# Kernel optimization log

Measured on AMD Instinct MI355X. Metric: run time of the kernel, lower is better.

Reference implementation:

```python
import jax, jax.numpy as jnp
import numpy as np

B, H, S, D = 4, 16, 2048, 64
MASK_FILL = 1e-12  # module quirk: masked scores set to 1e-12, not -inf


def setup_inputs() -> dict:
    key = jax.random.key(0)
    kq, kk, kv, km = jax.random.split(key, 4)
    q = jax.random.normal(kq, (B, H, S, D), dtype=jnp.float32)
    k = jax.random.normal(kk, (B, H, S, D), dtype=jnp.float32)
    v = jax.random.normal(kv, (B, H, S, D), dtype=jnp.float32)
    mask = jax.random.randint(km, (B, 1, 1, S), 0, 2, dtype=jnp.int32)
    return {"q": q, "k": k, "v": v, "mask": mask}


def reference(q, k, v, mask):
    dim = k.shape[-1]
    # scores: [B,H,S,S]
    scores = jnp.einsum('bhid,bhjd->bhij', q, k) * (dim ** -0.5)
    # faithful to masked_fill(mask == 0, 1e-12)
    scores = jnp.where(mask == 0, jnp.asarray(MASK_FILL, scores.dtype), scores)
    attention = jax.nn.softmax(scores, axis=-1)
    output = jnp.einsum('bhij,bhjd->bhid', attention, v)
    return output, attention
```

## Files before the change

### kernel.cpp

```cpp
#include <hip/hip_runtime.h>
#include <hip/hip_bf16.h>

namespace {

constexpr int S = 2048;
constexpr int D = 64;
constexpr float QSCALE = 0.125f * 1.4426950408889634f;

typedef __bf16 bf16x8 __attribute__((ext_vector_type(8)));
typedef float f32x16 __attribute__((ext_vector_type(16)));

#if __has_builtin(__builtin_amdgcn_exp2f)
__device__ __forceinline__ float fexp2(float x) { return __builtin_amdgcn_exp2f(x); }
#else
__device__ __forceinline__ float fexp2(float x) { return exp2f(x); }
#endif

__device__ __forceinline__ bf16x8 cvt8s(float4 a, float4 b, float s) {
    bf16x8 f;
    f[0] = (__bf16)(a.x * s); f[1] = (__bf16)(a.y * s);
    f[2] = (__bf16)(a.z * s); f[3] = (__bf16)(a.w * s);
    f[4] = (__bf16)(b.x * s); f[5] = (__bf16)(b.y * s);
    f[6] = (__bf16)(b.z * s); f[7] = (__bf16)(b.w * s);
    return f;
}
__device__ __forceinline__ bf16x8 cvt8(float4 a, float4 b) {
    bf16x8 f;
    f[0] = (__bf16)a.x; f[1] = (__bf16)a.y;
    f[2] = (__bf16)a.z; f[3] = (__bf16)a.w;
    f[4] = (__bf16)b.x; f[5] = (__bf16)b.y;
    f[6] = (__bf16)b.z; f[7] = (__bf16)b.w;
    return f;
}
__device__ __forceinline__ unsigned int pkbf(float lo, float hi) {
    unsigned int a = (unsigned int)__builtin_bit_cast(unsigned short, (__bf16)lo);
    unsigned int b = (unsigned int)__builtin_bit_cast(unsigned short, (__bf16)hi);
    return a | (b << 16);
}

}

__global__ void __launch_bounds__(256, 4)
attn_fused(const float* __restrict__ qg, const float* __restrict__ kg,
           const float* __restrict__ vg, const int* __restrict__ mg,
           float* __restrict__ og, float* __restrict__ ag)
{
    __shared__ bf16x8 kstage[2][256];
    __shared__ bf16x8 vstage[2][256];
    __shared__ unsigned int mlds[64];

    const int tid  = threadIdx.x;
    const int lane = tid & 63;
    const int w    = tid >> 6;
    const int l31  = lane & 31;
    const int h2   = lane >> 5;

    const int wid = (blockIdx.x & 7) * 128 + (blockIdx.x >> 3);
    const int bh  = wid >> 4;
    const int q0  = ((wid & 15) * 4 + w) * 32;
    const int b   = bh >> 4;

    const float* qrow = qg + ((size_t)bh * S + q0 + l31) * D + 8 * h2;
    const float* vb_  = vg + (size_t)bh * S * D;
    float* att  = ag + (size_t)bh * S * S + (size_t)q0 * S;
    float* orow = og + ((size_t)bh * S + q0) * D;

    const int srow  = tid >> 3;
    const int scol  = tid & 7;
    const int sslot = srow * 8 + (scol ^ (srow & 7));
    const float* ksrc = kg + (size_t)bh * S * D + (size_t)srow * D + scol * 8;
    int kslot[4];
#pragma unroll
    for (int t = 0; t < 4; ++t)
        kslot[t] = l31 * 8 + ((2 * t + h2) ^ (l31 & 7));

    const int vd = tid & 63;
    const int vw = tid >> 6;
    const int vwslot = vd * 4 + (vw ^ ((vd >> 1) & 3));
    const float* vsrc = vb_ + vd;
    int vslot[2][2];
#pragma unroll
    for (int f = 0; f < 2; ++f)
#pragma unroll
        for (int g = 0; g < 2; ++g) {
            const int d = l31 + 32 * g;
            vslot[f][g] = d * 4 + ((2 * f + h2) ^ ((d >> 1) & 3));
        }

    bf16x8 qa[4];
#pragma unroll
    for (int t = 0; t < 4; ++t) {
        const float4* p4 = (const float4*)(qrow + 16 * t);
        qa[t] = cvt8s(p4[0], p4[1], QSCALE);
    }

    if (tid < 64) {
        const int4* mp = (const int4*)(mg + (size_t)b * S + 32 * tid);
        unsigned int bits = 0;
#pragma unroll
        for (int k = 0; k < 8; ++k) {
            int4 m = mp[k];
            bits |= (unsigned int)(m.x != 0) << (4 * k);
            bits |= (unsigned int)(m.y != 0) << (4 * k + 1);
            bits |= (unsigned int)(m.z != 0) << (4 * k + 2);
            bits |= (unsigned int)(m.w != 0) << (4 * k + 3);
        }
        mlds[tid] = bits;
    }

    {
        const float4* p4 = (const float4*)ksrc;
        kstage[0][sslot] = cvt8(p4[0], p4[1]);
        bf16x8 vv;
#pragma unroll
        for (int k = 0; k < 8; ++k)
            vv[k] = (__bf16)vsrc[(size_t)(8 * vw + k) * D];
        vstage[0][vwslot] = vv;
    }
    __syncthreads();

    float ssum = 0.f;
    f32x16 oacc[2];
#pragma unroll
    for (int g = 0; g < 2; ++g)
#pragma unroll
        for (int r = 0; r < 16; ++r) oacc[g][r] = 0.f;

    int cur = 0;
    for (int j0 = 0; j0 < S; j0 += 32) {
        const bool more = (j0 + 32) < S;
        float4 kna{}, knb{};
        float vp[8];
        if (more) {
            const float4* p4 = (const float4*)(ksrc + (size_t)(j0 + 32) * D);
            kna = p4[0]; knb = p4[1];
#pragma unroll
            for (int k = 0; k < 8; ++k)
                vp[k] = vsrc[(size_t)(j0 + 32 + 8 * vw + k) * D];
        }
        const unsigned int mw = mlds[j0 >> 5];

        f32x16 acc;
#pragma unroll
        for (int r = 0; r < 16; ++r) acc[r] = 0.f;
        __builtin_amdgcn_s_setprio(1);
#pragma unroll
        for (int t = 0; t < 4; ++t)
            acc = __builtin_amdgcn_mfma_f32_32x32x16_bf16(kstage[cur][kslot[t]], qa[t], acc, 0, 0, 0);
        __builtin_amdgcn_s_setprio(0);

        const unsigned int mq = mw >> (4 * h2);
        unsigned int pk[8];
#pragma unroll
        for (int qd = 0; qd < 4; ++qd) {
            float pv[4];
#pragma unroll
            for (int i = 0; i < 4; ++i) {
                const float e = fexp2(acc[4 * qd + i]);
                pv[i] = ((mq >> (i + 8 * qd)) & 1) ? e : 1.0f;
                ssum += pv[i];
            }
            pk[2 * qd]     = pkbf(pv[0], pv[1]);
            pk[2 * qd + 1] = pkbf(pv[2], pv[3]);
        }
        asm volatile("v_permlane32_swap_b32 %0, %1" : "+v"(pk[0]), "+v"(pk[2]));
        asm volatile("v_permlane32_swap_b32 %0, %1" : "+v"(pk[1]), "+v"(pk[3]));
        asm volatile("v_permlane32_swap_b32 %0, %1" : "+v"(pk[4]), "+v"(pk[6]));
        asm volatile("v_permlane32_swap_b32 %0, %1" : "+v"(pk[5]), "+v"(pk[7]));
        typedef unsigned int uint4v __attribute__((ext_vector_type(4)));
        uint4v u0 = {pk[0], pk[1], pk[2], pk[3]};
        uint4v u1 = {pk[4], pk[5], pk[6], pk[7]};
        bf16x8 pa[2];
        pa[0] = __builtin_bit_cast(bf16x8, u0);
        pa[1] = __builtin_bit_cast(bf16x8, u1);

        __builtin_amdgcn_s_setprio(1);
#pragma unroll
        for (int f = 0; f < 2; ++f)
#pragma unroll
            for (int g = 0; g < 2; ++g)
                oacc[g] = __builtin_amdgcn_mfma_f32_32x32x16_bf16(pa[f], vstage[cur][vslot[f][g]], oacc[g], 0, 0, 0);
        __builtin_amdgcn_s_setprio(0);

        if (more) {
            kstage[cur ^ 1][sslot] = cvt8(kna, knb);
            bf16x8 vv;
#pragma unroll
            for (int k = 0; k < 8; ++k) vv[k] = (__bf16)vp[k];
            vstage[cur ^ 1][vwslot] = vv;
        }
        __syncthreads();
        cur ^= 1;
    }

    const float inv = 1.0f / (ssum + __shfl_xor(ssum, 32));
    float invq[16];
#pragma unroll
    for (int r = 0; r < 16; ++r)
        invq[r] = __shfl(inv, (r & 3) + 8 * (r >> 2) + 4 * h2);

#pragma unroll
    for (int g = 0; g < 2; ++g)
#pragma unroll
        for (int r = 0; r < 16; ++r) {
            const int qr = (r & 3) + 8 * (r >> 2) + 4 * h2;
            __builtin_nontemporal_store(oacc[g][r] * invq[r],
                                        &orow[(size_t)qr * D + 32 * g + l31]);
        }

    {
        const float4* p4 = (const float4*)ksrc;
        kstage[0][sslot] = cvt8(p4[0], p4[1]);
    }
    __syncthreads();

    cur = 0;
    for (int j0 = 0; j0 < S; j0 += 32) {
        const bool more = (j0 + 32) < S;
        float4 kna{}, knb{};
        if (more) {
            const float4* p4 = (const float4*)(ksrc + (size_t)(j0 + 32) * D);
            kna = p4[0]; knb = p4[1];
        }
        const bool mf = (mlds[j0 >> 5] >> l31) & 1;

        f32x16 acc;
#pragma unroll
        for (int r = 0; r < 16; ++r) acc[r] = 0.f;
        __builtin_amdgcn_s_setprio(1);
#pragma unroll
        for (int t = 0; t < 4; ++t)
            acc = __builtin_amdgcn_mfma_f32_32x32x16_bf16(qa[t], kstage[cur][kslot[t]], acc, 0, 0, 0);
        __builtin_amdgcn_s_setprio(0);

#pragma unroll
        for (int r = 0; r < 16; ++r) {
            float p = mf ? fexp2(acc[r]) : 1.0f;
            p *= invq[r];
            const int qr = (r & 3) + 8 * (r >> 2) + 4 * h2;
            __builtin_nontemporal_store(p, &att[(size_t)qr * S + j0 + l31]);
        }
        if (more) kstage[cur ^ 1][sslot] = cvt8(kna, knb);
        __syncthreads();
        cur ^= 1;
    }
}

extern "C" void kernel_launch(void* const* d_in, const int* in_sizes, int n_in,
                              void* d_out, int out_size, void* d_ws, size_t ws_size,
                              hipStream_t stream) {
    const float* q    = (const float*)d_in[0];
    const float* k    = (const float*)d_in[1];
    const float* v    = (const float*)d_in[2];
    const int*   mask = (const int*)d_in[3];
    float* out = (float*)d_out;
    float* att = out + (size_t)64 * S * D;
    dim3 grid(1024), block(256);
    hipLaunchKernelGGL(attn_fused, grid, block, 0, stream,
                       q, k, v, mask, out, att);
}
```

Baseline: 291.9 us.

## Deepen K/V prefetch to two tiles ahead with triple-buffered LDS

```diff
diff --git a/kernel.cpp b/kernel.cpp
--- a/kernel.cpp
+++ b/kernel.cpp
@@ -5,10 +5,12 @@
 
 constexpr int S = 2048;
 constexpr int D = 64;
+constexpr int NT = S / 32;
 constexpr float QSCALE = 0.125f * 1.4426950408889634f;
 
 typedef __bf16 bf16x8 __attribute__((ext_vector_type(8)));
 typedef float f32x16 __attribute__((ext_vector_type(16)));
+typedef unsigned int uint32x4 __attribute__((ext_vector_type(4)));
 
 #if __has_builtin(__builtin_amdgcn_exp2f)
 __device__ __forceinline__ float fexp2(float x) { return __builtin_amdgcn_exp2f(x); }
@@ -45,8 +47,8 @@
            const float* __restrict__ vg, const int* __restrict__ mg,
            float* __restrict__ og, float* __restrict__ ag)
 {
-    __shared__ bf16x8 kstage[2][256];
-    __shared__ bf16x8 vstage[2][256];
+    __shared__ bf16x8 kstage[3][256];
+    __shared__ bf16x8 vstage[3][256];
     __shared__ unsigned int mlds[64];
 
     const int tid  = threadIdx.x;
@@ -117,9 +119,18 @@
             vv[k] = (__bf16)vsrc[(size_t)(8 * vw + k) * D];
         vstage[0][vwslot] = vv;
     }
+    float4 k1a, k1b;
+    float  v1[8];
+    {
+        const float4* p4 = (const float4*)(ksrc + (size_t)32 * D);
+        k1a = p4[0]; k1b = p4[1];
+#pragma unroll
+        for (int k = 0; k < 8; ++k)
+            v1[k] = vsrc[(size_t)(32 + 8 * vw + k) * D];
+    }
     __syncthreads();
 
-    float ssum = 0.f;
+    float sums4[4] = {0.f, 0.f, 0.f, 0.f};
     f32x16 oacc[2];
 #pragma unroll
     for (int g = 0; g < 2; ++g)
@@ -127,29 +138,31 @@
         for (int r = 0; r < 16; ++r) oacc[g][r] = 0.f;
 
     int cur = 0;
-    for (int j0 = 0; j0 < S; j0 += 32) {
-        const bool more = (j0 + 32) < S;
-        float4 kna{}, knb{};
-        float vp[8];
-        if (more) {
-            const float4* p4 = (const float4*)(ksrc + (size_t)(j0 + 32) * D);
-            kna = p4[0]; knb = p4[1];
+    for (int t = 0; t < NT; ++t) {
+        const int j0  = t * 32;
+        const int nxt = (cur == 2) ? 0 : cur + 1;
+
+        float4 k2a{}, k2b{};
+        float  v2[8];
+        const bool have2 = (t + 2) < NT;
+        if (have2) {
+            const float4* p4 = (const float4*)(ksrc + (size_t)(j0 + 64) * D);
+            k2a = p4[0]; k2b = p4[1];
 #pragma unroll
             for (int k = 0; k < 8; ++k)
-                vp[k] = vsrc[(size_t)(j0 + 32 + 8 * vw + k) * D];
-        }
-        const unsigned int mw = mlds[j0 >> 5];
+                v2[k] = vsrc[(size_t)(j0 + 64 + 8 * vw + k) * D];
+        }
 
         f32x16 acc;
 #pragma unroll
         for (int r = 0; r < 16; ++r) acc[r] = 0.f;
         __builtin_amdgcn_s_setprio(1);
 #pragma unroll
-        for (int t = 0; t < 4; ++t)
-            acc = __builtin_amdgcn_mfma_f32_32x32x16_bf16(kstage[cur][kslot[t]], qa[t], acc, 0, 0, 0);
+        for (int u = 0; u < 4; ++u)
+            acc = __builtin_amdgcn_mfma_f32_32x32x16_bf16(kstage[cur][kslot[u]], qa[u], acc, 0, 0, 0);
         __builtin_amdgcn_s_setprio(0);
 
-        const unsigned int mq = mw >> (4 * h2);
+        const unsigned int mq = mlds[j0 >> 5] >> (4 * h2);
         unsigned int pk[8];
 #pragma unroll
         for (int qd = 0; qd < 4; ++qd) {
@@ -158,7 +171,7 @@
             for (int i = 0; i < 4; ++i) {
                 const float e = fexp2(acc[4 * qd + i]);
                 pv[i] = ((mq >> (i + 8 * qd)) & 1) ? e : 1.0f;
-                ssum += pv[i];
+                sums4[qd] += pv[i];
             }
             pk[2 * qd]     = pkbf(pv[0], pv[1]);
             pk[2 * qd + 1] = pkbf(pv[2], pv[3]);
@@ -167,9 +180,8 @@
         asm volatile("v_permlane32_swap_b32 %0, %1" : "+v"(pk[1]), "+v"(pk[3]));
         asm volatile("v_permlane32_swap_b32 %0, %1" : "+v"(pk[4]), "+v"(pk[6]));
         asm volatile("v_permlane32_swap_b32 %0, %1" : "+v"(pk[5]), "+v"(pk[7]));
-        typedef unsigned int uint4v __attribute__((ext_vector_type(4)));
-        uint4v u0 = {pk[0], pk[1], pk[2], pk[3]};
-        uint4v u1 = {pk[4], pk[5], pk[6], pk[7]};
+        uint32x4 u0 = {pk[0], pk[1], pk[2], pk[3]};
+        uint32x4 u1 = {pk[4], pk[5], pk[6], pk[7]};
         bf16x8 pa[2];
         pa[0] = __builtin_bit_cast(bf16x8, u0);
         pa[1] = __builtin_bit_cast(bf16x8, u1);
@@ -182,17 +194,22 @@
                 oacc[g] = __builtin_amdgcn_mfma_f32_32x32x16_bf16(pa[f], vstage[cur][vslot[f][g]], oacc[g], 0, 0, 0);
         __builtin_amdgcn_s_setprio(0);
 
-        if (more) {
-            kstage[cur ^ 1][sslot] = cvt8(kna, knb);
+        if ((t + 1) < NT) {
+            kstage[nxt][sslot] = cvt8(k1a, k1b);
             bf16x8 vv;
 #pragma unroll
-            for (int k = 0; k < 8; ++k) vv[k] = (__bf16)vp[k];
-            vstage[cur ^ 1][vwslot] = vv;
+            for (int k = 0; k < 8; ++k) vv[k] = (__bf16)v1[k];
+            vstage[nxt][vwslot] = vv;
         }
         __syncthreads();
-        cur ^= 1;
-    }
-
+
+        k1a = k2a; k1b = k2b;
+#pragma unroll
+        for (int k = 0; k < 8; ++k) v1[k] = v2[k];
+        cur = nxt;
+    }
+
+    const float ssum = (sums4[0] + sums4[1]) + (sums4[2] + sums4[3]);
     const float inv = 1.0f / (ssum + __shfl_xor(ssum, 32));
     float invq[16];
 #pragma unroll
@@ -229,8 +246,8 @@
         for (int r = 0; r < 16; ++r) acc[r] = 0.f;
         __builtin_amdgcn_s_setprio(1);
 #pragma unroll
-        for (int t = 0; t < 4; ++t)
-            acc = __builtin_amdgcn_mfma_f32_32x32x16_bf16(qa[t], kstage[cur][kslot[t]], acc, 0, 0, 0);
+        for (int u = 0; u < 4; ++u)
+            acc = __builtin_amdgcn_mfma_f32_32x32x16_bf16(qa[u], kstage[cur][kslot[u]], acc, 0, 0, 0);
         __builtin_amdgcn_s_setprio(0);
 
 #pragma unroll
@@ -255,7 +272,6 @@
     const int*   mask = (const int*)d_in[3];
     float* out = (float*)d_out;
     float* att = out + (size_t)64 * S * D;
-    dim3 grid(1024), block(256);
-    hipLaunchKernelGGL(attn_fused, grid, block, 0, stream,
+    hipLaunchKernelGGL(attn_fused, dim3(1024), dim3(256), 0, stream,
                        q, k, v, mask, out, att);
 }
```

Result: no change. 289.6 us (-0.8%).
